# Performance work log

Hardware: AMD Instinct MI355X
Metric: run time of the kernel (lower is better)

The kernel has to match this reference:

```python
import jax, jax.numpy as jnp
import numpy as np

TWO_PI = 2.0 * np.pi
SIGMA_EPS = 0.01
SIGMA_DIR = 0.001


def _means_sigmas(latents):
    # latents: [M, 6]
    means = latents[:, :4]  # [M, 4] (mean_x, mean_y, mean_dir_x, mean_dir_y)
    sigma_x = jax.nn.relu(latents[:, 4]) + SIGMA_EPS
    sigma_y = jax.nn.relu(latents[:, 5]) + SIGMA_EPS
    sigma_dir = jnp.full((latents.shape[0],), SIGMA_DIR, dtype=latents.dtype)
    sigmas = jnp.stack([sigma_x, sigma_y, sigma_dir, sigma_dir], axis=-1)  # [M, 4]
    return means, sigmas


def setup_inputs() -> dict:
    key = jax.random.key(0)
    k1, k2, k3 = jax.random.split(key, 3)
    N, M = 65536, 512
    return {
        "origins": jax.random.normal(k1, (N, 2), dtype=jnp.float32),
        "directions": jax.random.normal(k2, (N, 2), dtype=jnp.float32),
        "latents": jax.random.normal(k3, (M, 6), dtype=jnp.float32),
    }


def reference(origins, directions, latents):
    pos = jnp.concatenate([origins, directions], axis=1)  # [N, 4]
    means, sigmas = _means_sigmas(latents)  # [M, 4] each
    D = pos.shape[1]  # 4

    # pdf_max per gaussian: 1 / ((2*pi)^(d/2) * sqrt(prod(sigma)))
    det = jnp.prod(sigmas, axis=-1)  # [M]
    norm = (TWO_PI ** (D / 2)) * jnp.sqrt(det)  # [M]
    pdf_max = 1.0 / norm  # [M]

    # broadcast NxM pdf evaluation (diff/exponent intermediates are [N, M, 4])
    diff = pos[:, None, :] - means[None, :, :]  # [N, M, 4]
    exponent = -0.5 * jnp.sum(diff * diff / sigmas[None, :, :], axis=-1)  # [N, M]
    pdf = jnp.exp(exponent) / norm[None, :]  # [N, M]

    gaussian_values = pdf / pdf_max[None, :]  # [N, M]
    prob = jnp.clip(jnp.sum(gaussian_values, axis=1), 0.0, 1.0)  # [N]
    return prob.reshape(-1, 1)
```

## Files before the change

### kernel.cpp

```cpp
#include <hip/hip_runtime.h>

#if __has_builtin(__builtin_amdgcn_exp2f)
#define EXP2F(x) __builtin_amdgcn_exp2f(x)
#else
#define EXP2F(x) exp2f(x)
#endif

typedef float v2f __attribute__((ext_vector_type(2)));

constexpr float L2E = 1.4426950408889634f;
constexpr float CD  = -500.0f * L2E;
#define MAXP 256

static __device__ __forceinline__ v2f mk2(float x, float y) {
    v2f r; r.x = x; r.y = y; return r;
}

__global__ __launch_bounds__(512, 8)
void decoder_fused(const float* __restrict__ origins,
                   const float* __restrict__ directions,
                   const float* __restrict__ latents,
                   float* __restrict__ out, int N, int M, int P)
{
    __shared__ float4 lcf[MAXP * 4];
    __shared__ float  psum[512];

    const int tid = threadIdx.x;

    if (tid < P) {
        float c[2][7];
        #pragma unroll
        for (int h = 0; h < 2; ++h) {
            int j = 2 * tid + h;
            if (j < M) {
                const float* L = latents + j * 6;
                float mx = L[0], my = L[1], mdx = L[2], mdy = L[3];
                float A = (-0.5f * L2E) / (fmaxf(L[4], 0.0f) + 0.01f);
                float B = (-0.5f * L2E) / (fmaxf(L[5], 0.0f) + 0.01f);
                c[h][0] = A;
                c[h][1] = B;
                c[h][2] = -2.0f * A * mx;
                c[h][3] = -2.0f * B * my;
                c[h][4] = -2.0f * CD * mdx;
                c[h][5] = -2.0f * CD * mdy;
                c[h][6] = A*mx*mx + B*my*my + CD*(mdx*mdx + mdy*mdy);
            } else {
                c[h][0] = c[h][1] = c[h][2] = c[h][3] = c[h][4] = c[h][5] = 0.0f;
                c[h][6] = -3.0e38f;
            }
        }
        lcf[tid*4 + 0] = make_float4(c[0][0], c[1][0], c[0][1], c[1][1]);
        lcf[tid*4 + 1] = make_float4(c[0][2], c[1][2], c[0][3], c[1][3]);
        lcf[tid*4 + 2] = make_float4(c[0][4], c[1][4], c[0][5], c[1][5]);
        lcf[tid*4 + 3] = make_float4(c[0][6], c[1][6], 0.0f, 0.0f);
    }

    const int lane = tid & 63;
    const int part = tid >> 6;
    const int i    = blockIdx.x * 64 + lane;
    const int ii   = (i < N) ? i : (N > 0 ? N - 1 : 0);

    const float2 o = ((const float2*)origins)[ii];
    const float2 d = ((const float2*)directions)[ii];
    const float K  = CD * fmaf(d.y, d.y, d.x * d.x);
    const v2f px2 = mk2(o.x, o.x), py2 = mk2(o.y, o.y);
    const v2f qx2 = mk2(o.x*o.x, o.x*o.x), qy2 = mk2(o.y*o.y, o.y*o.y);
    const v2f dx2 = mk2(d.x, d.x), dy2 = mk2(d.y, d.y);
    const v2f K2  = mk2(K, K);

    __syncthreads();

    const int chunk = (P + 7) >> 3;
    int pb = part * chunk;
    int pe = pb + chunk; if (pe > P) pe = P;
    pb = __builtin_amdgcn_readfirstlane(pb);
    pe = __builtin_amdgcn_readfirstlane(pe);

    v2f acc0 = mk2(0.0f, 0.0f), acc1 = mk2(0.0f, 0.0f);

    #pragma unroll 2
    for (int p = pb; p < pe; ++p) {
        float4 a0 = lcf[4*p + 0];
        float4 a1 = lcf[4*p + 1];
        float4 a2 = lcf[4*p + 2];
        float4 a3 = lcf[4*p + 3];
        v2f e = mk2(a3.x, a3.y) + K2;
        e = __builtin_elementwise_fma(mk2(a0.x, a0.y), qx2, e);
        e = __builtin_elementwise_fma(mk2(a0.z, a0.w), qy2, e);
        e = __builtin_elementwise_fma(mk2(a1.x, a1.y), px2, e);
        e = __builtin_elementwise_fma(mk2(a1.z, a1.w), py2, e);
        e = __builtin_elementwise_fma(mk2(a2.x, a2.y), dx2, e);
        e = __builtin_elementwise_fma(mk2(a2.z, a2.w), dy2, e);
        v2f x = mk2(EXP2F(e.x), EXP2F(e.y));
        if (p & 1) acc1 += x; else acc0 += x;
    }

    v2f accs = acc0 + acc1;
    psum[tid] = accs.x + accs.y;
    __syncthreads();

    if (tid < 64 && i < N) {
        float t = 0.0f;
        #pragma unroll
        for (int k = 0; k < 8; ++k) t += psum[lane + 64*k];
        out[i] = fminf(fmaxf(t, 0.0f), 1.0f);
    }
}

extern "C" void kernel_launch(void* const* d_in, const int* in_sizes, int n_in,
                              void* d_out, int out_size, void* d_ws, size_t ws_size,
                              hipStream_t stream) {
    const float* origins    = (const float*)d_in[0];
    const float* directions = (const float*)d_in[1];
    const float* latents    = (const float*)d_in[2];
    float* out = (float*)d_out;

    int N = in_sizes[0] / 2;
    int M = in_sizes[2] / 6;
    if (M > 2 * MAXP) M = 2 * MAXP;
    int P = (M + 1) / 2;

    int nblocks = (N + 63) / 64;
    decoder_fused<<<nblocks, 512, 0, stream>>>(origins, directions, latents,
                                               out, N, M, P);
}
```

Measured before the change: 16.45 us.

## Process four point tiles per block to reuse shared-memory Gaussian coefficients

Each block now handles 256 points instead of 64: every thread keeps four points' terms in registers and evaluates each Gaussian coefficient pair loaded from LDS against all four. This spreads the LDS loads and the per-block coefficient setup over four times as many points, and the grid shrinks to a quarter of the blocks. In exchange register pressure rises (launch bounds relaxed to 4 waves per SIMD), the partial-sum buffer grows, and the smaller grid (256 blocks) may underfill the GPU.

```diff
diff --git a/kernel.cpp b/kernel.cpp
--- a/kernel.cpp
+++ b/kernel.cpp
@@ -16,14 +16,14 @@
     v2f r; r.x = x; r.y = y; return r;
 }
 
-__global__ __launch_bounds__(512, 8)
+__global__ __launch_bounds__(512, 4)
 void decoder_fused(const float* __restrict__ origins,
                    const float* __restrict__ directions,
                    const float* __restrict__ latents,
                    float* __restrict__ out, int N, int M, int P)
 {
     __shared__ float4 lcf[MAXP * 4];
-    __shared__ float  psum[512];
+    __shared__ float  psum[8 * 256];
 
     const int tid = threadIdx.x;
 
@@ -57,16 +57,21 @@
 
     const int lane = tid & 63;
     const int part = tid >> 6;
-    const int i    = blockIdx.x * 64 + lane;
-    const int ii   = (i < N) ? i : (N > 0 ? N - 1 : 0);
+    const int base = blockIdx.x * 256;
 
-    const float2 o = ((const float2*)origins)[ii];
-    const float2 d = ((const float2*)directions)[ii];
-    const float K  = CD * fmaf(d.y, d.y, d.x * d.x);
-    const v2f px2 = mk2(o.x, o.x), py2 = mk2(o.y, o.y);
-    const v2f qx2 = mk2(o.x*o.x, o.x*o.x), qy2 = mk2(o.y*o.y, o.y*o.y);
-    const v2f dx2 = mk2(d.x, d.x), dy2 = mk2(d.y, d.y);
-    const v2f K2  = mk2(K, K);
+    v2f px[4], py[4], qx[4], qy[4], dxv[4], dyv[4], Kv[4];
+    #pragma unroll
+    for (int t = 0; t < 4; ++t) {
+        int i  = base + t * 64 + lane;
+        int ii = (i < N) ? i : (N > 0 ? N - 1 : 0);
+        float2 o = ((const float2*)origins)[ii];
+        float2 d = ((const float2*)directions)[ii];
+        px[t] = mk2(o.x, o.x); py[t] = mk2(o.y, o.y);
+        qx[t] = px[t] * px[t]; qy[t] = py[t] * py[t];
+        dxv[t] = mk2(d.x, d.x); dyv[t] = mk2(d.y, d.y);
+        float K = CD * fmaf(d.y, d.y, d.x * d.x);
+        Kv[t] = mk2(K, K);
+    }
 
     __syncthreads();
 
@@ -76,7 +81,9 @@
     pb = __builtin_amdgcn_readfirstlane(pb);
     pe = __builtin_amdgcn_readfirstlane(pe);
 
-    v2f acc0 = mk2(0.0f, 0.0f), acc1 = mk2(0.0f, 0.0f);
+    v2f acc[4];
+    #pragma unroll
+    for (int t = 0; t < 4; ++t) acc[t] = mk2(0.0f, 0.0f);
 
     #pragma unroll 2
     for (int p = pb; p < pe; ++p) {
@@ -84,26 +91,37 @@
         float4 a1 = lcf[4*p + 1];
         float4 a2 = lcf[4*p + 2];
         float4 a3 = lcf[4*p + 3];
-        v2f e = mk2(a3.x, a3.y) + K2;
-        e = __builtin_elementwise_fma(mk2(a0.x, a0.y), qx2, e);
-        e = __builtin_elementwise_fma(mk2(a0.z, a0.w), qy2, e);
-        e = __builtin_elementwise_fma(mk2(a1.x, a1.y), px2, e);
-        e = __builtin_elementwise_fma(mk2(a1.z, a1.w), py2, e);
-        e = __builtin_elementwise_fma(mk2(a2.x, a2.y), dx2, e);
-        e = __builtin_elementwise_fma(mk2(a2.z, a2.w), dy2, e);
-        v2f x = mk2(EXP2F(e.x), EXP2F(e.y));
-        if (p & 1) acc1 += x; else acc0 += x;
+        v2f w0 = mk2(a0.x, a0.y), w1 = mk2(a0.z, a0.w);
+        v2f w2 = mk2(a1.x, a1.y), w3 = mk2(a1.z, a1.w);
+        v2f w4 = mk2(a2.x, a2.y), w5 = mk2(a2.z, a2.w);
+        v2f w6 = mk2(a3.x, a3.y);
+
+        #pragma unroll
+        for (int t = 0; t < 4; ++t) {
+            v2f e = w6 + Kv[t];
+            e = __builtin_elementwise_fma(w0, qx[t],  e);
+            e = __builtin_elementwise_fma(w1, qy[t],  e);
+            e = __builtin_elementwise_fma(w2, px[t],  e);
+            e = __builtin_elementwise_fma(w3, py[t],  e);
+            e = __builtin_elementwise_fma(w4, dxv[t], e);
+            e = __builtin_elementwise_fma(w5, dyv[t], e);
+            acc[t] += mk2(EXP2F(e.x), EXP2F(e.y));
+        }
     }
 
-    v2f accs = acc0 + acc1;
-    psum[tid] = accs.x + accs.y;
+    #pragma unroll
+    for (int t = 0; t < 4; ++t)
+        psum[part * 256 + t * 64 + lane] = acc[t].x + acc[t].y;
     __syncthreads();
 
-    if (tid < 64 && i < N) {
-        float t = 0.0f;
-        #pragma unroll
-        for (int k = 0; k < 8; ++k) t += psum[lane + 64*k];
-        out[i] = fminf(fmaxf(t, 0.0f), 1.0f);
+    if (tid < 256) {
+        int i = base + tid;
+        if (i < N) {
+            float t = 0.0f;
+            #pragma unroll
+            for (int k = 0; k < 8; ++k) t += psum[k * 256 + tid];
+            out[i] = fminf(fmaxf(t, 0.0f), 1.0f);
+        }
     }
 }
 
@@ -120,7 +138,7 @@
     if (M > 2 * MAXP) M = 2 * MAXP;
     int P = (M + 1) / 2;
 
-    int nblocks = (N + 63) / 64;
+    int nblocks = (N + 255) / 256;
     decoder_fused<<<nblocks, 512, 0, stream>>>(origins, directions, latents,
                                                out, N, M, P);
 }
```

Result: faster. 15.05 us (-8.5%).
